# Kernel tuning notes

Measured on AMD Instinct MI355X. Metric: run time of the kernel, lower is better.

Reference implementation:

```python
import jax, jax.numpy as jnp
import numpy as np

L = 12      # n_blocks
H = 12      # n_heads
V = 64      # val_dim
D = 768     # hidden_d (token dim)
MLP = 3072  # MLP_dim
NP = 14     # n_patches per side
PS = 16     # patch size
C = 3       # channels
NC = 1000   # num_classes
EPS = 1e-5  # LayerNorm eps


def pos_embeddings(S, d):
    # result[i,j] = sin(i/10000**(j/d)) if j even else cos(i/10000**((j-1)/d))
    i = jnp.arange(S, dtype=jnp.float32)[:, None]
    j = jnp.arange(d, dtype=jnp.float32)[None, :]
    angle = i / jnp.power(10000.0, (j - (j % 2)) / d)
    even = (jnp.arange(d) % 2) == 0
    return jnp.where(even[None, :], jnp.sin(angle), jnp.cos(angle))


def patchify(images):
    # [n,C,H,W] -> [n, NP*NP, C*PS*PS], patch flattened in (c, ph, pw) order
    n = images.shape[0]
    x = images.reshape(n, C, NP, PS, NP, PS)
    x = x.transpose(0, 2, 4, 1, 3, 5)  # n, i, j, c, ps, ps
    return x.reshape(n, NP * NP, C * PS * PS)


def layernorm(x, w, b):
    m = jnp.mean(x, axis=-1, keepdims=True)
    v = jnp.var(x, axis=-1, keepdims=True)
    return (x - m) * jax.lax.rsqrt(v + EPS) * w + b


def setup_inputs() -> dict:
    key = jax.random.key(0)
    ks = jax.random.split(key, 10)
    s = lambda k, shape, scale=0.02: jax.random.normal(k, shape, jnp.float32) * scale
    return {
        "images": jax.random.normal(ks[0], (32, C, NP * PS, NP * PS), jnp.float32),
        "W_map": s(ks[1], (C * PS * PS, D)),          # linear_mapper (no bias)
        "class_token": s(ks[2], (1, D), 1.0),
        "pos_emb": pos_embeddings(NP * NP + 1, D),     # buffer
        "ln1_w": jnp.ones((L, D)), "ln1_b": jnp.zeros((L, D)),
        "qkv_w": s(ks[3], (L, D, 3 * H * V)),          # to_qkv (no bias)
        "merge_w": s(ks[4], (L, H * V, D)),            # Merge (no bias)
        "ln2_w": jnp.ones((L, D)), "ln2_b": jnp.zeros((L, D)),
        "mlp_w1": s(ks[5], (L, D, MLP)), "mlp_b1": jnp.zeros((L, MLP)),
        "mlp_w2": s(ks[6], (L, MLP, D)), "mlp_b2": jnp.zeros((L, D)),
        "head_w": s(ks[7], (D, NC)), "head_b": jnp.zeros((NC,)),
    }


def reference(images, W_map, class_token, pos_emb, ln1_w, ln1_b, qkv_w,
              merge_w, ln2_w, ln2_b, mlp_w1, mlp_b1, mlp_w2, mlp_b2,
              head_w, head_b):
    n = images.shape[0]
    tokens = patchify(images) @ W_map                              # [n, P, D]
    tokens = jnp.concatenate([jnp.broadcast_to(class_token, (n, 1, D)), tokens], axis=1)
    x = tokens + pos_emb                                           # [n, P+1, D]

    def block(x, p):
        l1w, l1b, qw, mw, l2w, l2b, w1, b1, w2, b2 = p
        h = layernorm(x, l1w, l1b)
        # rearrange 'b p (h v k) -> k b h p v' (k innermost factor)
        qkv = (h @ qw).reshape(n, -1, H, V, 3)
        q, k, v = qkv[..., 0], qkv[..., 1], qkv[..., 2]            # [n, P+1, H, V]
        attn = jnp.einsum('bihd,bjhd->bhij', q, k) * (V ** -0.5)
        attn = jax.nn.softmax(attn, axis=-1)
        o = jnp.einsum('bhij,bjhd->bihd', attn, v).reshape(n, -1, H * V)
        x = x + o @ mw
        h2 = layernorm(x, l2w, l2b)
        x = x + (jax.nn.gelu(h2 @ w1 + b1, approximate=False) @ w2 + b2)
        return x, None

    x, _ = jax.lax.scan(block, x, (ln1_w, ln1_b, qkv_w, merge_w,
                                   ln2_w, ln2_b, mlp_w1, mlp_b1, mlp_w2, mlp_b2))
    return jax.nn.softmax(x[:, 0] @ head_w + head_b, axis=-1)      # [n, NC]
```

## Files before the change

kernel.cpp:

```cpp
#include <hip/hip_runtime.h>
#include <math.h>

#define NIMG 32
#define NP2  196
#define PTOK 197
#define DIM  768
#define NH   12
#define VD   64
#define MLPD 3072
#define ROWS (NIMG*PTOK)
#define PROWS (NIMG*NP2)
#define MPAD 6400
#define PSTR 208
#define BHN (NIMG*NH)

typedef float f32x4 __attribute__((ext_vector_type(4)));
typedef short bf16x8 __attribute__((ext_vector_type(8)));
typedef unsigned short u16x8 __attribute__((ext_vector_type(8)));
typedef unsigned short u16x4 __attribute__((ext_vector_type(4)));

__device__ __forceinline__ unsigned short f2bf(float x) {
    unsigned int u = __float_as_uint(x);
    return (unsigned short)((u + 0x7FFFu + ((u >> 16) & 1u)) >> 16);
}
__device__ __forceinline__ float bfhi(unsigned short h) {
    return __uint_as_float(((unsigned int)h) << 16);
}
__device__ __forceinline__ void glds16(const unsigned short* g, unsigned short* l) {
    __builtin_amdgcn_global_load_lds(
        (const __attribute__((address_space(1))) unsigned int*)g,
        (__attribute__((address_space(3))) unsigned int*)l, 16, 0, 0);
}

__global__ __launch_bounds__(256) void patchify_kernel(const float* __restrict__ img,
                                                       unsigned short* __restrict__ ph,
                                                       unsigned short* __restrict__ pl)
{
    int idx = blockIdx.x * 256 + threadIdx.x;
    if (idx >= PROWS * DIM) return;
    int row = idx / DIM, kk = idx % DIM;
    int b = row / NP2, p = row % NP2;
    int i = p / 14, j = p % 14;
    int c = kk >> 8, r = kk & 255;
    int pr = r >> 4, pw = r & 15;
    float v = img[(((size_t)b*3 + c)*224 + i*16 + pr)*224 + j*16 + pw];
    unsigned short hi = f2bf(v);
    ph[idx] = hi;
    pl[idx] = f2bf(v - bfhi(hi));
}

__global__ __launch_bounds__(256) void class_pos_kernel(const float* __restrict__ ct,
                                                        const float* __restrict__ pos,
                                                        float* __restrict__ x)
{
    int idx = blockIdx.x * 256 + threadIdx.x;
    if (idx >= NIMG * DIM) return;
    int b = idx / DIM, d = idx % DIM;
    x[(size_t)b * PTOK * DIM + d] = ct[d] + pos[d];
}

__device__ __forceinline__ void conv_body(const float* __restrict__ W,
    unsigned short* __restrict__ Bh, unsigned short* __restrict__ Bl, int K, int N)
{
    int idx = blockIdx.x * 256 + threadIdx.x;
    if (idx >= N * (K >> 5)) return;
    int kb = idx / N;
    int n  = idx - kb * N;
    size_t off = (((size_t)(n >> 7) * (K >> 5) + kb) * 128 + (n & 127)) * 32;
    #pragma unroll
    for (int u = 0; u < 4; ++u) {
        u16x8 h, l;
        #pragma unroll
        for (int j = 0; j < 8; ++j) {
            float x = W[(size_t)(kb * 32 + u * 8 + j) * N + n];
            unsigned short hh = f2bf(x);
            h[j] = hh;
            l[j] = f2bf(x - bfhi(hh));
        }
        *(u16x8*)&Bh[off + u * 8] = h;
        *(u16x8*)&Bl[off + u * 8] = l;
    }
}

__global__ __launch_bounds__(256) void convert_one(const float* __restrict__ W,
    unsigned short* __restrict__ Bh, unsigned short* __restrict__ Bl, int K, int N)
{
    conv_body(W, Bh, Bl, K, N);
}

__global__ __launch_bounds__(256) void convert_layer(
    const float* __restrict__ qw, const float* __restrict__ mw,
    const float* __restrict__ w1, const float* __restrict__ w2,
    unsigned short* qh, unsigned short* ql, unsigned short* mh, unsigned short* ml,
    unsigned short* h1, unsigned short* l1, unsigned short* h2, unsigned short* l2)
{
    switch (blockIdx.y) {
        case 0: conv_body(qw, qh, ql, DIM, 3*NH*VD); break;
        case 1: conv_body(mw, mh, ml, DIM, DIM);     break;
        case 2: conv_body(w1, h1, l1, DIM, MLPD);    break;
        case 3: conv_body(w2, h2, l2, MLPD, DIM);    break;
    }
}

template<int MODE>
__global__ __launch_bounds__(512, 4) void mgemm(
    const unsigned short* __restrict__ Ah, const unsigned short* __restrict__ Al,
    const unsigned short* __restrict__ Bh, const unsigned short* __restrict__ Bl,
    float* __restrict__ C, int M, int N, int K, int gm, int gn,
    const float* __restrict__ bias, const float* __restrict__ res,
    const float* __restrict__ pos,
    unsigned int* __restrict__ qo, unsigned int* __restrict__ ko, unsigned int* __restrict__ vo,
    unsigned short* __restrict__ oph, unsigned short* __restrict__ opl)
{
    __shared__ unsigned short SAh[256 * 32];
    __shared__ unsigned short SAl[256 * 32];
    __shared__ unsigned short SBh[128 * 32];
    __shared__ unsigned short SBl[128 * 32];

    const int tid = threadIdx.x;
    const int nwg = gm * gn;
    const int q = nwg >> 3, r = nwg & 7;
    const int xcd = blockIdx.x & 7, li = blockIdx.x >> 3;
    const int seq = xcd * q + (xcd < r ? xcd : r) + li;
    const int mt = seq / gn, nt = seq - mt * gn;
    const int m0 = mt * 256, n0 = nt * 128;

    const int wave = tid >> 6, lane = tid & 63;
    const int wm = (wave >> 1) * 64, wn = (wave & 1) * 64;
    const int lr = lane & 15, lg = lane >> 4;

    const int r0 = tid >> 2, sl = tid & 3;
    const int s0 = sl ^ ((r0 >> 1) & 3);
    const size_t aoff0 = (size_t)(m0 + r0) * K + s0 * 8;
    const size_t aoff1 = (size_t)(m0 + r0 + 128) * K + s0 * 8;
    const size_t boff0 = (size_t)(n0 >> 7) * (K >> 5) * 4096 + (size_t)r0 * 32 + s0 * 8;

    int aro[4], bro[4];
    #pragma unroll
    for (int i = 0; i < 4; ++i) {
        int rowA = wm + i * 16 + lr;
        aro[i] = rowA * 32 + ((lg ^ ((rowA >> 1) & 3)) * 8);
        int rowB = wn + i * 16 + lr;
        bro[i] = rowB * 32 + ((lg ^ ((rowB >> 1) & 3)) * 8);
    }

    f32x4 acc[4][4];
    #pragma unroll
    for (int i = 0; i < 4; ++i)
        #pragma unroll
        for (int j = 0; j < 4; ++j)
            #pragma unroll
            for (int e = 0; e < 4; ++e) acc[i][j][e] = 0.f;

    const int kSteps = K >> 5;
    #pragma unroll 1
    for (int ks = 0; ks < kSteps; ++ks) {
        __syncthreads();
        const size_t ak = (size_t)ks * 32;
        const size_t bk = (size_t)ks * 4096;
        glds16(Ah + aoff0 + ak, SAh + tid * 8);
        glds16(Ah + aoff1 + ak, SAh + 4096 + tid * 8);
        glds16(Al + aoff0 + ak, SAl + tid * 8);
        glds16(Al + aoff1 + ak, SAl + 4096 + tid * 8);
        glds16(Bh + boff0 + bk, SBh + tid * 8);
        glds16(Bl + boff0 + bk, SBl + tid * 8);
        __syncthreads();

        bf16x8 bfh[4], bfl[4];
        #pragma unroll
        for (int ni = 0; ni < 4; ++ni) {
            bfh[ni] = *(const bf16x8*)&SBh[bro[ni]];
            bfl[ni] = *(const bf16x8*)&SBl[bro[ni]];
        }
        #pragma unroll
        for (int mi = 0; mi < 4; ++mi) {
            bf16x8 afh = *(const bf16x8*)&SAh[aro[mi]];
            bf16x8 afl = *(const bf16x8*)&SAl[aro[mi]];
            #pragma unroll
            for (int ni = 0; ni < 4; ++ni) {
                acc[mi][ni] = __builtin_amdgcn_mfma_f32_16x16x32_bf16(afh, bfh[ni], acc[mi][ni], 0, 0, 0);
                acc[mi][ni] = __builtin_amdgcn_mfma_f32_16x16x32_bf16(afh, bfl[ni], acc[mi][ni], 0, 0, 0);
                acc[mi][ni] = __builtin_amdgcn_mfma_f32_16x16x32_bf16(afl, bfh[ni], acc[mi][ni], 0, 0, 0);
            }
        }
    }

    #pragma unroll
    for (int mi = 0; mi < 4; ++mi) {
        #pragma unroll
        for (int ni = 0; ni < 4; ++ni) {
            f32x4 v = acc[mi][ni];
            int c = n0 + wn + ni * 16 + lr;
            #pragma unroll
            for (int rr = 0; rr < 4; ++rr) {
                int r = m0 + wm + mi * 16 + lg * 4 + rr;
                if (r >= M) continue;
                float val = v[rr];
                if (MODE == 1) {
                    int b = r / NP2, p = r - b * NP2;
                    C[((size_t)b * PTOK + 1 + p) * DIM + c] = val + pos[(size_t)(p + 1) * DIM + c];
                } else if (MODE == 2) {
                    int b = r / PTOK, p = r - b * PTOK;
                    int t = c % 3, hv = c / 3;
                    int hd = hv >> 6, vv = hv & 63;
                    size_t bh = (size_t)b * NH + hd;
                    float sv = (t == 0) ? val * 0.125f : val;
                    unsigned short hi = f2bf(sv);
                    unsigned short lo = f2bf(sv - bfhi(hi));
                    unsigned int w32 = (unsigned int)hi | ((unsigned int)lo << 16);
                    if (t == 2) vo[(bh * 64 + vv) * PSTR + p] = w32;
                    else if (t == 0) qo[(bh * PSTR + p) * 64 + vv] = w32;
                    else ko[(bh * PSTR + p) * 64 + vv] = w32;
                } else if (MODE == 3) {
                    float tmp = val + bias[c];
                    float gel = 0.5f * tmp * (1.0f + erff(tmp * 0.70710678118654752f));
                    unsigned short hi = f2bf(gel);
                    oph[(size_t)r * N + c] = hi;
                    opl[(size_t)r * N + c] = f2bf(gel - bfhi(hi));
                } else if (MODE == 4) {
                    C[(size_t)r * N + c] = res[(size_t)r * N + c] + val;
                } else if (MODE == 5) {
                    C[(size_t)r * N + c] = res[(size_t)r * N + c] + val + bias[c];
                }
            }
        }
    }
}

__global__ __launch_bounds__(256) void ln_kernel(const float* __restrict__ x,
                                                 const float* __restrict__ w,
                                                 const float* __restrict__ b,
                                                 unsigned short* __restrict__ oh,
                                                 unsigned short* __restrict__ ol, int rows)
{
    int wave = threadIdx.x >> 6, lane = threadIdx.x & 63;
    int row = blockIdx.x * 4 + wave;
    if (row >= rows) return;
    const float* xr = x + (size_t)row * DIM;
    float vals[12];
    float sum = 0.f;
    #pragma unroll
    for (int u = 0; u < 12; ++u) { vals[u] = xr[u * 64 + lane]; sum += vals[u]; }
    #pragma unroll
    for (int off = 32; off; off >>= 1) sum += __shfl_xor(sum, off);
    float mean = sum * (1.f / DIM);
    float vs = 0.f;
    #pragma unroll
    for (int u = 0; u < 12; ++u) { float d = vals[u] - mean; vs += d * d; }
    #pragma unroll
    for (int off = 32; off; off >>= 1) vs += __shfl_xor(vs, off);
    float rstd = rsqrtf(vs * (1.f / DIM) + 1e-5f);
    #pragma unroll
    for (int u = 0; u < 12; ++u) {
        int d = u * 64 + lane;
        float v = (vals[u] - mean) * rstd * w[d] + b[d];
        unsigned short hi = f2bf(v);
        oh[(size_t)row * DIM + d] = hi;
        ol[(size_t)row * DIM + d] = f2bf(v - bfhi(hi));
    }
}

__global__ __launch_bounds__(256) void attn_mfma(
    const unsigned int* __restrict__ qp, const unsigned int* __restrict__ kp,
    const unsigned int* __restrict__ vtp,
    unsigned short* __restrict__ oh, unsigned short* __restrict__ ol)
{
    __shared__ unsigned short KVh[64 * 72];
    __shared__ unsigned short KVl[64 * 72];
    __shared__ unsigned short Ph[64 * 72];
    __shared__ unsigned short Pl[64 * 72];

    const int tid = threadIdx.x;
    const int w = tid >> 6, lane = tid & 63;
    const int l = lane & 15, g = lane >> 4;
    const int bh = blockIdx.y, q0 = blockIdx.x * 64;
    const int b = bh / NH, hd = bh - b * NH;

    int qrow = q0 + 16 * w + l;
    if (qrow >= PTOK) qrow = 0;
    const unsigned int* qbase = qp + ((size_t)bh * PSTR + qrow) * 64;
    bf16x8 qAh[2], qAl[2];
    #pragma unroll
    for (int ks = 0; ks < 2; ++ks) {
        const unsigned int* p = qbase + 32 * ks + 8 * g;
        uint4 a = *(const uint4*)p;
        uint4 c = *(const uint4*)(p + 4);
        bf16x8 h8, l8;
        h8[0]=(short)a.x; h8[1]=(short)a.y; h8[2]=(short)a.z; h8[3]=(short)a.w;
        h8[4]=(short)c.x; h8[5]=(short)c.y; h8[6]=(short)c.z; h8[7]=(short)c.w;
        l8[0]=(short)(a.x>>16); l8[1]=(short)(a.y>>16); l8[2]=(short)(a.z>>16); l8[3]=(short)(a.w>>16);
        l8[4]=(short)(c.x>>16); l8[5]=(short)(c.y>>16); l8[6]=(short)(c.z>>16); l8[7]=(short)(c.w>>16);
        qAh[ks] = h8; qAl[ks] = l8;
    }

    f32x4 s[13];
    #pragma unroll
    for (int t = 0; t < 13; ++t)
        #pragma unroll
        for (int e = 0; e < 4; ++e) s[t][e] = 0.f;

    for (int c = 0; c < 4; ++c) {
        __syncthreads();
        const int rows = (c < 3) ? 64 : 16;
        for (int u = tid; u < rows * 16; u += 256) {
            int r = u >> 4, cc = u & 15;
            int j = c * 64 + r;
            uint4 wv = make_uint4(0, 0, 0, 0);
            if (j < PTOK) wv = *(const uint4*)(kp + ((size_t)bh * PSTR + j) * 64 + cc * 4);
            u16x4 h4, l4;
            h4[0]=(unsigned short)wv.x; h4[1]=(unsigned short)wv.y;
            h4[2]=(unsigned short)wv.z; h4[3]=(unsigned short)wv.w;
            l4[0]=(unsigned short)(wv.x>>16); l4[1]=(unsigned short)(wv.y>>16);
            l4[2]=(unsigned short)(wv.z>>16); l4[3]=(unsigned short)(wv.w>>16);
            *(u16x4*)&KVh[r * 72 + cc * 4] = h4;
            *(u16x4*)&KVl[r * 72 + cc * 4] = l4;
        }
        __syncthreads();
        const int tc = (c < 3) ? 4 : 1;
        for (int t = 0; t < tc; ++t) {
            int ti = c * 4 + t;
            #pragma unroll
            for (int ks = 0; ks < 2; ++ks) {
                bf16x8 kh = *(const bf16x8*)&KVh[(16 * t + l) * 72 + 32 * ks + 8 * g];
                bf16x8 kl = *(const bf16x8*)&KVl[(16 * t + l) * 72 + 32 * ks + 8 * g];
                s[ti] = __builtin_amdgcn_mfma_f32_16x16x32_bf16(qAh[ks], kh, s[ti], 0, 0, 0);
                s[ti] = __builtin_amdgcn_mfma_f32_16x16x32_bf16(qAh[ks], kl, s[ti], 0, 0, 0);
                s[ti] = __builtin_amdgcn_mfma_f32_16x16x32_bf16(qAl[ks], kh, s[ti], 0, 0, 0);
            }
        }
    }

    if (l >= 5) {
        #pragma unroll
        for (int e = 0; e < 4; ++e) s[12][e] = -1e30f;
    }

    float mx[4], rs[4];
    #pragma unroll
    for (int e = 0; e < 4; ++e) {
        float m = s[0][e];
        #pragma unroll
        for (int t = 1; t < 13; ++t) m = fmaxf(m, s[t][e]);
        #pragma unroll
        for (int off = 1; off < 16; off <<= 1) m = fmaxf(m, __shfl_xor(m, off));
        mx[e] = m;
    }
    #pragma unroll
    for (int e = 0; e < 4; ++e) {
        float sum = 0.f;
        #pragma unroll
        for (int t = 0; t < 13; ++t) {
            float p = __expf(s[t][e] - mx[e]);
            s[t][e] = p;
            sum += p;
        }
        #pragma unroll
        for (int off = 1; off < 16; off <<= 1) sum += __shfl_xor(sum, off);
        rs[e] = 1.f / sum;
    }

    f32x4 o[4];
    #pragma unroll
    for (int t = 0; t < 4; ++t)
        #pragma unroll
        for (int e = 0; e < 4; ++e) o[t][e] = 0.f;

    for (int c = 0; c < 4; ++c) {
        __syncthreads();
        const int cols = (c < 3) ? 64 : 32;
        const int cpr = cols >> 2;
        for (int u = tid; u < 64 * cpr; u += 256) {
            int r = u / cpr, cc = u % cpr;
            int jbase = c * 64 + cc * 4;
            uint4 wv;
            if (c < 3) {
                wv = *(const uint4*)(vtp + ((size_t)bh * 64 + r) * PSTR + jbase);
            } else {
                unsigned int t0 = (jbase + 0 < PTOK) ? vtp[((size_t)bh * 64 + r) * PSTR + jbase + 0] : 0u;
                unsigned int t1 = (jbase + 1 < PTOK) ? vtp[((size_t)bh * 64 + r) * PSTR + jbase + 1] : 0u;
                unsigned int t2 = (jbase + 2 < PTOK) ? vtp[((size_t)bh * 64 + r) * PSTR + jbase + 2] : 0u;
                unsigned int t3 = (jbase + 3 < PTOK) ? vtp[((size_t)bh * 64 + r) * PSTR + jbase + 3] : 0u;
                wv = make_uint4(t0, t1, t2, t3);
            }
            u16x4 h4, l4;
            h4[0]=(unsigned short)wv.x; h4[1]=(unsigned short)wv.y;
            h4[2]=(unsigned short)wv.z; h4[3]=(unsigned short)wv.w;
            l4[0]=(unsigned short)(wv.x>>16); l4[1]=(unsigned short)(wv.y>>16);
            l4[2]=(unsigned short)(wv.z>>16); l4[3]=(unsigned short)(wv.w>>16);
            *(u16x4*)&KVh[r * 72 + cc * 4] = h4;
            *(u16x4*)&KVl[r * 72 + cc * 4] = l4;
        }
        const int tc = (c < 3) ? 4 : 1;
        for (int t = 0; t < tc; ++t) {
            int ti = c * 4 + t;
            #pragma unroll
            for (int e = 0; e < 4; ++e) {
                int row = 16 * w + 4 * g + e, col = 16 * t + l;
                float pv = s[ti][e];
                unsigned short hi = f2bf(pv);
                Ph[row * 72 + col] = hi;
                Pl[row * 72 + col] = f2bf(pv - bfhi(hi));
            }
        }
        __syncthreads();
        const int ksn = (c < 3) ? 2 : 1;
        for (int ks = 0; ks < ksn; ++ks) {
            bf16x8 pa_h = *(const bf16x8*)&Ph[(16 * w + l) * 72 + 32 * ks + 8 * g];
            bf16x8 pa_l = *(const bf16x8*)&Pl[(16 * w + l) * 72 + 32 * ks + 8 * g];
            #pragma unroll
            for (int tv = 0; tv < 4; ++tv) {
                bf16x8 vh = *(const bf16x8*)&KVh[(16 * tv + l) * 72 + 32 * ks + 8 * g];
                bf16x8 vl = *(const bf16x8*)&KVl[(16 * tv + l) * 72 + 32 * ks + 8 * g];
                o[tv] = __builtin_amdgcn_mfma_f32_16x16x32_bf16(pa_h, vh, o[tv], 0, 0, 0);
                o[tv] = __builtin_amdgcn_mfma_f32_16x16x32_bf16(pa_h, vl, o[tv], 0, 0, 0);
                o[tv] = __builtin_amdgcn_mfma_f32_16x16x32_bf16(pa_l, vh, o[tv], 0, 0, 0);
            }
        }
    }

    #pragma unroll
    for (int tv = 0; tv < 4; ++tv) {
        #pragma unroll
        for (int e = 0; e < 4; ++e) {
            int q = q0 + 16 * w + 4 * g + e;
            if (q < PTOK) {
                float v = o[tv][e] * rs[e];
                size_t idx = ((size_t)(b * PTOK + q)) * DIM + hd * 64 + 16 * tv + l;
                unsigned short hi = f2bf(v);
                oh[idx] = hi;
                ol[idx] = f2bf(v - bfhi(hi));
            }
        }
    }
}

__global__ __launch_bounds__(256) void head_kernel(const float* __restrict__ x,
                                                   const float* __restrict__ W,
                                                   const float* __restrict__ bias,
                                                   float* __restrict__ out)
{
    __shared__ __align__(16) float xl[DIM];
    __shared__ float red[4];
    int b = blockIdx.x;
    const float* xr = x + (size_t)b * PTOK * DIM;
    for (int idx = threadIdx.x; idx < DIM; idx += 256) xl[idx] = xr[idx];
    __syncthreads();

    float logit[4];
    #pragma unroll
    for (int u = 0; u < 4; ++u) {
        int c = threadIdx.x + u * 256;
        float acc = (c < 1000) ? bias[c] : -INFINITY;
        if (c < 1000) {
            for (int k = 0; k < DIM; k += 4) {
                float4 xv = *(const float4*)&xl[k];
                acc += xv.x * W[(size_t)k * 1000 + c]
                     + xv.y * W[(size_t)(k + 1) * 1000 + c]
                     + xv.z * W[(size_t)(k + 2) * 1000 + c]
                     + xv.w * W[(size_t)(k + 3) * 1000 + c];
            }
        }
        logit[u] = acc;
    }
    int lane = threadIdx.x & 63, wv = threadIdx.x >> 6;
    float m = fmaxf(fmaxf(logit[0], logit[1]), fmaxf(logit[2], logit[3]));
    #pragma unroll
    for (int off = 32; off; off >>= 1) m = fmaxf(m, __shfl_xor(m, off));
    if (lane == 0) red[wv] = m;
    __syncthreads();
    m = fmaxf(fmaxf(red[0], red[1]), fmaxf(red[2], red[3]));

    float p[4]; float sum = 0.f;
    #pragma unroll
    for (int u = 0; u < 4; ++u) {
        int c = threadIdx.x + u * 256;
        p[u] = (c < 1000) ? expf(logit[u] - m) : 0.f;
        sum += p[u];
    }
    #pragma unroll
    for (int off = 32; off; off >>= 1) sum += __shfl_xor(sum, off);
    __syncthreads();
    if (lane == 0) red[wv] = sum;
    __syncthreads();
    float inv = 1.f / (red[0] + red[1] + red[2] + red[3]);
    #pragma unroll
    for (int u = 0; u < 4; ++u) {
        int c = threadIdx.x + u * 256;
        if (c < 1000) out[(size_t)b * 1000 + c] = p[u] * inv;
    }
}

extern "C" void kernel_launch(void* const* d_in, const int* in_sizes, int n_in,
                              void* d_out, int out_size, void* d_ws, size_t ws_size,
                              hipStream_t stream)
{
    const float* images  = (const float*)d_in[0];
    const float* W_map   = (const float*)d_in[1];
    const float* ct      = (const float*)d_in[2];
    const float* pos     = (const float*)d_in[3];
    const float* ln1_w   = (const float*)d_in[4];
    const float* ln1_b   = (const float*)d_in[5];
    const float* qkv_w   = (const float*)d_in[6];
    const float* merge_w = (const float*)d_in[7];
    const float* ln2_w   = (const float*)d_in[8];
    const float* ln2_b   = (const float*)d_in[9];
    const float* mlp_w1  = (const float*)d_in[10];
    const float* mlp_b1  = (const float*)d_in[11];
    const float* mlp_w2  = (const float*)d_in[12];
    const float* mlp_b2  = (const float*)d_in[13];
    const float* head_w  = (const float*)d_in[14];
    const float* head_b  = (const float*)d_in[15];
    float* out = (float*)d_out;

    float* ws = (float*)d_ws;
    const size_t XE   = (size_t)ROWS * DIM;
    const size_t PLND = (size_t)MPAD * DIM;
    const size_t GPL  = (size_t)MPAD * MLPD;

    float* x = ws;
    unsigned short* hh = (unsigned short*)(x + XE);
    unsigned short* hl = hh + PLND;
    unsigned short* oh = hl + PLND;
    unsigned short* ol = oh + PLND;
    unsigned short* gh = ol + PLND;
    unsigned short* gl = gh + GPL;

    const size_t PL = (size_t)BHN * PSTR * 64;
    unsigned int* qpl = (unsigned int*)gh;
    unsigned int* kpl = qpl + PL;
    unsigned int* vtp = kpl + PL;
    unsigned short* pph = gh;
    unsigned short* ppl = pph + PLND;

    unsigned short* wb = gl + GPL;
    const size_t qkvE = (size_t)DIM * 2304;
    const size_t mgE  = (size_t)DIM * DIM;
    const size_t m1E  = (size_t)DIM * MLPD;
    const size_t m2E  = (size_t)MLPD * DIM;
    unsigned short* qh  = wb;
    unsigned short* ql  = qh  + qkvE;
    unsigned short* mh  = ql  + qkvE;
    unsigned short* ml  = mh  + mgE;
    unsigned short* h1  = ml  + mgE;
    unsigned short* l1  = h1  + m1E;
    unsigned short* h2  = l1  + m1E;
    unsigned short* l2  = h2  + m2E;
    unsigned short* wmh = l2  + m2E;
    unsigned short* wml = wmh + mgE;

    patchify_kernel<<<(PROWS * DIM + 255) / 256, 256, 0, stream>>>(images, pph, ppl);
    class_pos_kernel<<<(NIMG * DIM + 255) / 256, 256, 0, stream>>>(ct, pos, x);
    convert_one<<<(DIM * (DIM / 32) + 255) / 256, 256, 0, stream>>>(W_map, wmh, wml, DIM, DIM);

    const int gm = 25;
    mgemm<1><<<gm * 6, 512, 0, stream>>>(
        pph, ppl, wmh, wml, x, PROWS, DIM, DIM, gm, 6,
        nullptr, nullptr, pos, nullptr, nullptr, nullptr, nullptr, nullptr);

    for (int l = 0; l < 12; ++l) {
        convert_layer<<<dim3(288, 4), 256, 0, stream>>>(
            qkv_w + (size_t)l * qkvE, merge_w + (size_t)l * mgE,
            mlp_w1 + (size_t)l * m1E, mlp_w2 + (size_t)l * m2E,
            qh, ql, mh, ml, h1, l1, h2, l2);
        ln_kernel<<<(ROWS + 3) / 4, 256, 0, stream>>>(x, ln1_w + l * DIM, ln1_b + l * DIM, hh, hl, ROWS);
        mgemm<2><<<gm * 18, 512, 0, stream>>>(
            hh, hl, qh, ql, nullptr, ROWS, 2304, DIM, gm, 18,
            nullptr, nullptr, nullptr, qpl, kpl, vtp, nullptr, nullptr);
        attn_mfma<<<dim3(4, BHN), 256, 0, stream>>>(qpl, kpl, vtp, oh, ol);
        mgemm<4><<<gm * 6, 512, 0, stream>>>(
            oh, ol, mh, ml, x, ROWS, DIM, DIM, gm, 6,
            nullptr, x, nullptr, nullptr, nullptr, nullptr, nullptr, nullptr);
        ln_kernel<<<(ROWS + 3) / 4, 256, 0, stream>>>(x, ln2_w + l * DIM, ln2_b + l * DIM, hh, hl, ROWS);
        mgemm<3><<<gm * 24, 512, 0, stream>>>(
            hh, hl, h1, l1, nullptr, ROWS, MLPD, DIM, gm, 24,
            mlp_b1 + (size_t)l * MLPD, nullptr, nullptr, nullptr, nullptr, nullptr, gh, gl);
        mgemm<5><<<gm * 6, 512, 0, stream>>>(
            gh, gl, h2, l2, x, ROWS, DIM, MLPD, gm, 6,
            mlp_b2 + (size_t)l * DIM, x, nullptr, nullptr, nullptr, nullptr, nullptr, nullptr);
    }
    head_kernel<<<NIMG, 256, 0, stream>>>(x, head_w, head_b, out);
}
```

Baseline: 6.507 ms.

## Double-buffer LDS in split-bf16 GEMM and shrink tile to 128x128 with 256 threads

The main GEMM kernel changes from a 256x128 tile with 512 threads and a single LDS buffer to a 128x128 tile with 256 threads and two LDS buffers. Global-to-LDS loads for the next K step are issued before the MFMA work on the current step, with one wait and barrier per step instead of two barriers. The goal is to hide global load latency behind MFMA work, and the smaller tiles give more workgroups for better CU fill. In exchange, each workgroup reuses less data, and the K-loop unrolled by two assumes an even number of K steps.

Result: no change. 6.427 ms (-1.2%).

```diff
diff --git a/kernel.cpp b/kernel.cpp
--- a/kernel.cpp
+++ b/kernel.cpp
@@ -103,7 +103,7 @@
 }
 
 template<int MODE>
-__global__ __launch_bounds__(512, 4) void mgemm(
+__global__ __launch_bounds__(256, 2) void mgemm(
     const unsigned short* __restrict__ Ah, const unsigned short* __restrict__ Al,
     const unsigned short* __restrict__ Bh, const unsigned short* __restrict__ Bl,
     float* __restrict__ C, int M, int N, int K, int gm, int gn,
@@ -112,10 +112,10 @@
     unsigned int* __restrict__ qo, unsigned int* __restrict__ ko, unsigned int* __restrict__ vo,
     unsigned short* __restrict__ oph, unsigned short* __restrict__ opl)
 {
-    __shared__ unsigned short SAh[256 * 32];
-    __shared__ unsigned short SAl[256 * 32];
-    __shared__ unsigned short SBh[128 * 32];
-    __shared__ unsigned short SBl[128 * 32];
+    __shared__ unsigned short SAh[2 * 4096];
+    __shared__ unsigned short SAl[2 * 4096];
+    __shared__ unsigned short SBh[2 * 4096];
+    __shared__ unsigned short SBl[2 * 4096];
 
     const int tid = threadIdx.x;
     const int nwg = gm * gn;
@@ -123,7 +123,7 @@
     const int xcd = blockIdx.x & 7, li = blockIdx.x >> 3;
     const int seq = xcd * q + (xcd < r ? xcd : r) + li;
     const int mt = seq / gn, nt = seq - mt * gn;
-    const int m0 = mt * 256, n0 = nt * 128;
+    const int m0 = mt * 128, n0 = nt * 128;
 
     const int wave = tid >> 6, lane = tid & 63;
     const int wm = (wave >> 1) * 64, wn = (wave & 1) * 64;
@@ -132,7 +132,7 @@
     const int r0 = tid >> 2, sl = tid & 3;
     const int s0 = sl ^ ((r0 >> 1) & 3);
     const size_t aoff0 = (size_t)(m0 + r0) * K + s0 * 8;
-    const size_t aoff1 = (size_t)(m0 + r0 + 128) * K + s0 * 8;
+    const size_t aoff1 = (size_t)(m0 + r0 + 64) * K + s0 * 8;
     const size_t boff0 = (size_t)(n0 >> 7) * (K >> 5) * 4096 + (size_t)r0 * 32 + s0 * 8;
 
     int aro[4], bro[4];
@@ -152,38 +152,68 @@
             #pragma unroll
             for (int e = 0; e < 4; ++e) acc[i][j][e] = 0.f;
 
+#define STAGE(KS, B) do { \
+    const size_t _ak = (size_t)(KS) * 32; \
+    const size_t _bk = (size_t)(KS) * 4096; \
+    unsigned short* _sah = SAh + (B) * 4096; \
+    unsigned short* _sal = SAl + (B) * 4096; \
+    unsigned short* _sbh = SBh + (B) * 4096; \
+    unsigned short* _sbl = SBl + (B) * 4096; \
+    glds16(Ah + aoff0 + _ak, _sah + tid * 8); \
+    glds16(Ah + aoff1 + _ak, _sah + 2048 + tid * 8); \
+    glds16(Al + aoff0 + _ak, _sal + tid * 8); \
+    glds16(Al + aoff1 + _ak, _sal + 2048 + tid * 8); \
+    glds16(Bh + boff0 + _bk, _sbh + tid * 8); \
+    glds16(Bh + boff0 + _bk + 2048, _sbh + 2048 + tid * 8); \
+    glds16(Bl + boff0 + _bk, _sbl + tid * 8); \
+    glds16(Bl + boff0 + _bk + 2048, _sbl + 2048 + tid * 8); \
+} while (0)
+
+#define COMPUTE(B) do { \
+    const unsigned short* _sah = SAh + (B) * 4096; \
+    const unsigned short* _sal = SAl + (B) * 4096; \
+    const unsigned short* _sbh = SBh + (B) * 4096; \
+    const unsigned short* _sbl = SBl + (B) * 4096; \
+    bf16x8 bfh[4], bfl[4]; \
+    _Pragma("unroll") \
+    for (int ni = 0; ni < 4; ++ni) { \
+        bfh[ni] = *(const bf16x8*)&_sbh[bro[ni]]; \
+        bfl[ni] = *(const bf16x8*)&_sbl[bro[ni]]; \
+    } \
+    _Pragma("unroll") \
+    for (int mi = 0; mi < 4; ++mi) { \
+        bf16x8 afh = *(const bf16x8*)&_sah[aro[mi]]; \
+        bf16x8 afl = *(const bf16x8*)&_sal[aro[mi]]; \
+        _Pragma("unroll") \
+        for (int ni = 0; ni < 4; ++ni) { \
+            acc[mi][ni] = __builtin_amdgcn_mfma_f32_16x16x32_bf16(afh, bfh[ni], acc[mi][ni], 0, 0, 0); \
+            acc[mi][ni] = __builtin_amdgcn_mfma_f32_16x16x32_bf16(afh, bfl[ni], acc[mi][ni], 0, 0, 0); \
+            acc[mi][ni] = __builtin_amdgcn_mfma_f32_16x16x32_bf16(afl, bfh[ni], acc[mi][ni], 0, 0, 0); \
+        } \
+    } \
+} while (0)
+
+#define WAITBAR do { \
+    asm volatile("s_waitcnt vmcnt(0)" ::: "memory"); \
+    __builtin_amdgcn_s_barrier(); \
+} while (0)
+
     const int kSteps = K >> 5;
+    STAGE(0, 0);
+    WAITBAR;
+
     #pragma unroll 1
-    for (int ks = 0; ks < kSteps; ++ks) {
-        __syncthreads();
-        const size_t ak = (size_t)ks * 32;
-        const size_t bk = (size_t)ks * 4096;
-        glds16(Ah + aoff0 + ak, SAh + tid * 8);
-        glds16(Ah + aoff1 + ak, SAh + 4096 + tid * 8);
-        glds16(Al + aoff0 + ak, SAl + tid * 8);
-        glds16(Al + aoff1 + ak, SAl + 4096 + tid * 8);
-        glds16(Bh + boff0 + bk, SBh + tid * 8);
-        glds16(Bl + boff0 + bk, SBl + tid * 8);
-        __syncthreads();
-
-        bf16x8 bfh[4], bfl[4];
-        #pragma unroll
-        for (int ni = 0; ni < 4; ++ni) {
-            bfh[ni] = *(const bf16x8*)&SBh[bro[ni]];
-            bfl[ni] = *(const bf16x8*)&SBl[bro[ni]];
-        }
-        #pragma unroll
-        for (int mi = 0; mi < 4; ++mi) {
-            bf16x8 afh = *(const bf16x8*)&SAh[aro[mi]];
-            bf16x8 afl = *(const bf16x8*)&SAl[aro[mi]];
-            #pragma unroll
-            for (int ni = 0; ni < 4; ++ni) {
-                acc[mi][ni] = __builtin_amdgcn_mfma_f32_16x16x32_bf16(afh, bfh[ni], acc[mi][ni], 0, 0, 0);
-                acc[mi][ni] = __builtin_amdgcn_mfma_f32_16x16x32_bf16(afh, bfl[ni], acc[mi][ni], 0, 0, 0);
-                acc[mi][ni] = __builtin_amdgcn_mfma_f32_16x16x32_bf16(afl, bfh[ni], acc[mi][ni], 0, 0, 0);
-            }
-        }
-    }
+    for (int ks = 0; ks < kSteps; ks += 2) {
+        STAGE(ks + 1, 1);
+        COMPUTE(0);
+        WAITBAR;
+        if (ks + 2 < kSteps) STAGE(ks + 2, 0);
+        COMPUTE(1);
+        WAITBAR;
+    }
+#undef STAGE
+#undef COMPUTE
+#undef WAITBAR
 
     #pragma unroll
     for (int mi = 0; mi < 4; ++mi) {
@@ -552,29 +582,30 @@
     class_pos_kernel<<<(NIMG * DIM + 255) / 256, 256, 0, stream>>>(ct, pos, x);
     convert_one<<<(DIM * (DIM / 32) + 255) / 256, 256, 0, stream>>>(W_map, wmh, wml, DIM, DIM);
 
-    const int gm = 25;
-    mgemm<1><<<gm * 6, 512, 0, stream>>>(
-        pph, ppl, wmh, wml, x, PROWS, DIM, DIM, gm, 6,
+    const int gme = 49;
+    mgemm<1><<<gme * 6, 256, 0, stream>>>(
+        pph, ppl, wmh, wml, x, PROWS, DIM, DIM, gme, 6,
         nullptr, nullptr, pos, nullptr, nullptr, nullptr, nullptr, nullptr);
 
+    const int gm = 50;
     for (int l = 0; l < 12; ++l) {
         convert_layer<<<dim3(288, 4), 256, 0, stream>>>(
             qkv_w + (size_t)l * qkvE, merge_w + (size_t)l * mgE,
             mlp_w1 + (size_t)l * m1E, mlp_w2 + (size_t)l * m2E,
             qh, ql, mh, ml, h1, l1, h2, l2);
         ln_kernel<<<(ROWS + 3) / 4, 256, 0, stream>>>(x, ln1_w + l * DIM, ln1_b + l * DIM, hh, hl, ROWS);
-        mgemm<2><<<gm * 18, 512, 0, stream>>>(
+        mgemm<2><<<gm * 18, 256, 0, stream>>>(
             hh, hl, qh, ql, nullptr, ROWS, 2304, DIM, gm, 18,
             nullptr, nullptr, nullptr, qpl, kpl, vtp, nullptr, nullptr);
         attn_mfma<<<dim3(4, BHN), 256, 0, stream>>>(qpl, kpl, vtp, oh, ol);
-        mgemm<4><<<gm * 6, 512, 0, stream>>>(
+        mgemm<4><<<gm * 6, 256, 0, stream>>>(
             oh, ol, mh, ml, x, ROWS, DIM, DIM, gm, 6,
             nullptr, x, nullptr, nullptr, nullptr, nullptr, nullptr, nullptr);
         ln_kernel<<<(ROWS + 3) / 4, 256, 0, stream>>>(x, ln2_w + l * DIM, ln2_b + l * DIM, hh, hl, ROWS);
-        mgemm<3><<<gm * 24, 512, 0, stream>>>(
+        mgemm<3><<<gm * 24, 256, 0, stream>>>(
             hh, hl, h1, l1, nullptr, ROWS, MLPD, DIM, gm, 24,
             mlp_b1 + (size_t)l * MLPD, nullptr, nullptr, nullptr, nullptr, nullptr, gh, gl);
-        mgemm<5><<<gm * 6, 512, 0, stream>>>(
+        mgemm<5><<<gm * 6, 256, 0, stream>>>(
             gh, gl, h2, l2, x, ROWS, DIM, MLPD, gm, 6,
             mlp_b2 + (size_t)l * DIM, x, nullptr, nullptr, nullptr, nullptr, nullptr, nullptr);
     }
```

## Add double-buffered 256x256 GEMM for wide layers, shrink narrow GEMM tiles

Applied to the files above, without the earlier changes.

Adds a new 512-thread GEMM kernel with 256x256 tiles and double-buffered LDS staging. The QKV and MLP-up projections now use it, giving each B tile more reuse and overlapping global-to-LDS loads with MFMA compute. The N=768 GEMMs (patch embed, merge, MLP-down) switch to 256-thread 128x128 tiles, doubling the workgroup count to fill more CUs. The large tile uses 128 KB of LDS and many accumulator registers, which limits occupancy. The smaller tile lowers per-block data reuse.

After: 6.182 ms. 5.0% less time.

```diff
diff --git a/kernel.cpp b/kernel.cpp
--- a/kernel.cpp
+++ b/kernel.cpp
@@ -103,7 +103,43 @@
 }
 
 template<int MODE>
-__global__ __launch_bounds__(512, 4) void mgemm(
+__device__ __forceinline__ void epi_store(
+    int r, int c, float val, float* __restrict__ C, int M, int N,
+    const float* __restrict__ bias, const float* __restrict__ res,
+    const float* __restrict__ pos,
+    unsigned int* __restrict__ qo, unsigned int* __restrict__ ko, unsigned int* __restrict__ vo,
+    unsigned short* __restrict__ oph, unsigned short* __restrict__ opl)
+{
+    if (MODE == 1) {
+        int b = r / NP2, p = r - b * NP2;
+        C[((size_t)b * PTOK + 1 + p) * DIM + c] = val + pos[(size_t)(p + 1) * DIM + c];
+    } else if (MODE == 2) {
+        int b = r / PTOK, p = r - b * PTOK;
+        int t = c % 3, hv = c / 3;
+        int hd = hv >> 6, vv = hv & 63;
+        size_t bh = (size_t)b * NH + hd;
+        float sv = (t == 0) ? val * 0.125f : val;
+        unsigned short hi = f2bf(sv);
+        unsigned short lo = f2bf(sv - bfhi(hi));
+        unsigned int w32 = (unsigned int)hi | ((unsigned int)lo << 16);
+        if (t == 2) vo[(bh * 64 + vv) * PSTR + p] = w32;
+        else if (t == 0) qo[(bh * PSTR + p) * 64 + vv] = w32;
+        else ko[(bh * PSTR + p) * 64 + vv] = w32;
+    } else if (MODE == 3) {
+        float tmp = val + bias[c];
+        float gel = 0.5f * tmp * (1.0f + erff(tmp * 0.70710678118654752f));
+        unsigned short hi = f2bf(gel);
+        oph[(size_t)r * N + c] = hi;
+        opl[(size_t)r * N + c] = f2bf(gel - bfhi(hi));
+    } else if (MODE == 4) {
+        C[(size_t)r * N + c] = res[(size_t)r * N + c] + val;
+    } else if (MODE == 5) {
+        C[(size_t)r * N + c] = res[(size_t)r * N + c] + val + bias[c];
+    }
+}
+
+template<int MODE>
+__global__ __launch_bounds__(256, 4) void mgemm(
     const unsigned short* __restrict__ Ah, const unsigned short* __restrict__ Al,
     const unsigned short* __restrict__ Bh, const unsigned short* __restrict__ Bl,
     float* __restrict__ C, int M, int N, int K, int gm, int gn,
@@ -112,10 +148,10 @@
     unsigned int* __restrict__ qo, unsigned int* __restrict__ ko, unsigned int* __restrict__ vo,
     unsigned short* __restrict__ oph, unsigned short* __restrict__ opl)
 {
-    __shared__ unsigned short SAh[256 * 32];
-    __shared__ unsigned short SAl[256 * 32];
-    __shared__ unsigned short SBh[128 * 32];
-    __shared__ unsigned short SBl[128 * 32];
+    __shared__ unsigned short SAh[4096];
+    __shared__ unsigned short SAl[4096];
+    __shared__ unsigned short SBh[4096];
+    __shared__ unsigned short SBl[4096];
 
     const int tid = threadIdx.x;
     const int nwg = gm * gn;
@@ -123,7 +159,7 @@
     const int xcd = blockIdx.x & 7, li = blockIdx.x >> 3;
     const int seq = xcd * q + (xcd < r ? xcd : r) + li;
     const int mt = seq / gn, nt = seq - mt * gn;
-    const int m0 = mt * 256, n0 = nt * 128;
+    const int m0 = mt * 128, n0 = nt * 128;
 
     const int wave = tid >> 6, lane = tid & 63;
     const int wm = (wave >> 1) * 64, wn = (wave & 1) * 64;
@@ -132,7 +168,7 @@
     const int r0 = tid >> 2, sl = tid & 3;
     const int s0 = sl ^ ((r0 >> 1) & 3);
     const size_t aoff0 = (size_t)(m0 + r0) * K + s0 * 8;
-    const size_t aoff1 = (size_t)(m0 + r0 + 128) * K + s0 * 8;
+    const size_t aoff1 = (size_t)(m0 + r0 + 64) * K + s0 * 8;
     const size_t boff0 = (size_t)(n0 >> 7) * (K >> 5) * 4096 + (size_t)r0 * 32 + s0 * 8;
 
     int aro[4], bro[4];
@@ -159,11 +195,13 @@
         const size_t ak = (size_t)ks * 32;
         const size_t bk = (size_t)ks * 4096;
         glds16(Ah + aoff0 + ak, SAh + tid * 8);
-        glds16(Ah + aoff1 + ak, SAh + 4096 + tid * 8);
+        glds16(Ah + aoff1 + ak, SAh + 2048 + tid * 8);
         glds16(Al + aoff0 + ak, SAl + tid * 8);
-        glds16(Al + aoff1 + ak, SAl + 4096 + tid * 8);
+        glds16(Al + aoff1 + ak, SAl + 2048 + tid * 8);
         glds16(Bh + boff0 + bk, SBh + tid * 8);
+        glds16(Bh + boff0 + bk + 2048, SBh + 2048 + tid * 8);
         glds16(Bl + boff0 + bk, SBl + tid * 8);
+        glds16(Bl + boff0 + bk + 2048, SBl + 2048 + tid * 8);
         __syncthreads();
 
         bf16x8 bfh[4], bfl[4];
@@ -193,35 +231,143 @@
             int c = n0 + wn + ni * 16 + lr;
             #pragma unroll
             for (int rr = 0; rr < 4; ++rr) {
-                int r = m0 + wm + mi * 16 + lg * 4 + rr;
-                if (r >= M) continue;
-                float val = v[rr];
-                if (MODE == 1) {
-                    int b = r / NP2, p = r - b * NP2;
-                    C[((size_t)b * PTOK + 1 + p) * DIM + c] = val + pos[(size_t)(p + 1) * DIM + c];
-                } else if (MODE == 2) {
-                    int b = r / PTOK, p = r - b * PTOK;
-                    int t = c % 3, hv = c / 3;
-                    int hd = hv >> 6, vv = hv & 63;
-                    size_t bh = (size_t)b * NH + hd;
-                    float sv = (t == 0) ? val * 0.125f : val;
-                    unsigned short hi = f2bf(sv);
-                    unsigned short lo = f2bf(sv - bfhi(hi));
-                    unsigned int w32 = (unsigned int)hi | ((unsigned int)lo << 16);
-                    if (t == 2) vo[(bh * 64 + vv) * PSTR + p] = w32;
-                    else if (t == 0) qo[(bh * PSTR + p) * 64 + vv] = w32;
-                    else ko[(bh * PSTR + p) * 64 + vv] = w32;
-                } else if (MODE == 3) {
-                    float tmp = val + bias[c];
-                    float gel = 0.5f * tmp * (1.0f + erff(tmp * 0.70710678118654752f));
-                    unsigned short hi = f2bf(gel);
-                    oph[(size_t)r * N + c] = hi;
-                    opl[(size_t)r * N + c] = f2bf(gel - bfhi(hi));
-                } else if (MODE == 4) {
-                    C[(size_t)r * N + c] = res[(size_t)r * N + c] + val;
-                } else if (MODE == 5) {
-                    C[(size_t)r * N + c] = res[(size_t)r * N + c] + val + bias[c];
-                }
+                int rr2 = m0 + wm + mi * 16 + lg * 4 + rr;
+                if (rr2 >= M) continue;
+                epi_store<MODE>(rr2, c, v[rr], C, M, N, bias, res, pos, qo, ko, vo, oph, opl);
+            }
+        }
+    }
+}
+
+template<int MODE>
+__global__ __launch_bounds__(512, 2) void mgemm2(
+    const unsigned short* __restrict__ Ah, const unsigned short* __restrict__ Al,
+    const unsigned short* __restrict__ Bh, const unsigned short* __restrict__ Bl,
+    float* __restrict__ C, int M, int N, int K, int gm, int gn,
+    const float* __restrict__ bias, const float* __restrict__ res,
+    const float* __restrict__ pos,
+    unsigned int* __restrict__ qo, unsigned int* __restrict__ ko, unsigned int* __restrict__ vo,
+    unsigned short* __restrict__ oph, unsigned short* __restrict__ opl)
+{
+    __shared__ unsigned short SAh[2 * 8192];
+    __shared__ unsigned short SAl[2 * 8192];
+    __shared__ unsigned short SBh[2 * 8192];
+    __shared__ unsigned short SBl[2 * 8192];
+
+    const int tid = threadIdx.x;
+    const int nwg = gm * gn;
+    const int q = nwg >> 3, r = nwg & 7;
+    const int xcd = blockIdx.x & 7, li = blockIdx.x >> 3;
+    const int seq = xcd * q + (xcd < r ? xcd : r) + li;
+    const int mt = seq / gn, nt = seq - mt * gn;
+    const int m0 = mt * 256, n0 = nt * 256;
+
+    const int wave = tid >> 6, lane = tid & 63;
+    const int wm = (wave >> 2) * 128, wn = (wave & 3) * 64;
+    const int lr = lane & 15, lg = lane >> 4;
+
+    const int r0 = tid >> 2, sl = tid & 3;
+    const int s0 = sl ^ ((r0 >> 1) & 3);
+    const size_t aoff0 = (size_t)(m0 + r0) * K + s0 * 8;
+    const size_t aoff1 = (size_t)(m0 + r0 + 128) * K + s0 * 8;
+    const size_t bstep = (size_t)(K >> 5) * 4096;
+    const size_t bo0 = (size_t)(n0 >> 7) * bstep + (size_t)r0 * 32 + s0 * 8;
+    const size_t bo1 = bo0 + bstep;
+
+    int aro[8], bro[4];
+    #pragma unroll
+    for (int i = 0; i < 8; ++i) {
+        int rowA = wm + i * 16 + lr;
+        aro[i] = rowA * 32 + ((lg ^ ((rowA >> 1) & 3)) * 8);
+    }
+    #pragma unroll
+    for (int i = 0; i < 4; ++i) {
+        int rowB = wn + i * 16 + lr;
+        bro[i] = rowB * 32 + ((lg ^ ((rowB >> 1) & 3)) * 8);
+    }
+
+    f32x4 acc[8][4];
+    #pragma unroll
+    for (int i = 0; i < 8; ++i)
+        #pragma unroll
+        for (int j = 0; j < 4; ++j)
+            #pragma unroll
+            for (int e = 0; e < 4; ++e) acc[i][j][e] = 0.f;
+
+#define STAGE2(KS, B) do { \
+    const size_t _ak = (size_t)(KS) * 32; \
+    const size_t _bk = (size_t)(KS) * 4096; \
+    unsigned short* _sah = SAh + (B) * 8192; \
+    unsigned short* _sal = SAl + (B) * 8192; \
+    unsigned short* _sbh = SBh + (B) * 8192; \
+    unsigned short* _sbl = SBl + (B) * 8192; \
+    glds16(Ah + aoff0 + _ak, _sah + tid * 8); \
+    glds16(Ah + aoff1 + _ak, _sah + 4096 + tid * 8); \
+    glds16(Al + aoff0 + _ak, _sal + tid * 8); \
+    glds16(Al + aoff1 + _ak, _sal + 4096 + tid * 8); \
+    glds16(Bh + bo0 + _bk, _sbh + tid * 8); \
+    glds16(Bh + bo1 + _bk, _sbh + 4096 + tid * 8); \
+    glds16(Bl + bo0 + _bk, _sbl + tid * 8); \
+    glds16(Bl + bo1 + _bk, _sbl + 4096 + tid * 8); \
+} while (0)
+
+#define COMPUTE2(B) do { \
+    const unsigned short* _sah = SAh + (B) * 8192; \
+    const unsigned short* _sal = SAl + (B) * 8192; \
+    const unsigned short* _sbh = SBh + (B) * 8192; \
+    const unsigned short* _sbl = SBl + (B) * 8192; \
+    bf16x8 bfh[4], bfl[4]; \
+    _Pragma("unroll") \
+    for (int ni = 0; ni < 4; ++ni) { \
+        bfh[ni] = *(const bf16x8*)&_sbh[bro[ni]]; \
+        bfl[ni] = *(const bf16x8*)&_sbl[bro[ni]]; \
+    } \
+    _Pragma("unroll") \
+    for (int mi = 0; mi < 8; ++mi) { \
+        bf16x8 afh = *(const bf16x8*)&_sah[aro[mi]]; \
+        bf16x8 afl = *(const bf16x8*)&_sal[aro[mi]]; \
+        _Pragma("unroll") \
+        for (int ni = 0; ni < 4; ++ni) { \
+            acc[mi][ni] = __builtin_amdgcn_mfma_f32_16x16x32_bf16(afh, bfh[ni], acc[mi][ni], 0, 0, 0); \
+            acc[mi][ni] = __builtin_amdgcn_mfma_f32_16x16x32_bf16(afh, bfl[ni], acc[mi][ni], 0, 0, 0); \
+            acc[mi][ni] = __builtin_amdgcn_mfma_f32_16x16x32_bf16(afl, bfh[ni], acc[mi][ni], 0, 0, 0); \
+        } \
+    } \
+} while (0)
+
+#define WAITBAR2 do { \
+    asm volatile("s_waitcnt vmcnt(0)" ::: "memory"); \
+    __builtin_amdgcn_s_barrier(); \
+} while (0)
+
+    const int kSteps = K >> 5;
+    STAGE2(0, 0);
+    WAITBAR2;
+
+    #pragma unroll 1
+    for (int ks = 0; ks < kSteps; ks += 2) {
+        STAGE2(ks + 1, 1);
+        COMPUTE2(0);
+        WAITBAR2;
+        if (ks + 2 < kSteps) STAGE2(ks + 2, 0);
+        COMPUTE2(1);
+        WAITBAR2;
+    }
+#undef STAGE2
+#undef COMPUTE2
+#undef WAITBAR2
+
+    #pragma unroll
+    for (int mi = 0; mi < 8; ++mi) {
+        #pragma unroll
+        for (int ni = 0; ni < 4; ++ni) {
+            f32x4 v = acc[mi][ni];
+            int c = n0 + wn + ni * 16 + lr;
+            #pragma unroll
+            for (int rr = 0; rr < 4; ++rr) {
+                int rr2 = m0 + wm + mi * 16 + lg * 4 + rr;
+                if (rr2 >= M) continue;
+                epi_store<MODE>(rr2, c, v[rr], C, M, N, bias, res, pos, qo, ko, vo, oph, opl);
             }
         }
     }
@@ -552,29 +698,31 @@
     class_pos_kernel<<<(NIMG * DIM + 255) / 256, 256, 0, stream>>>(ct, pos, x);
     convert_one<<<(DIM * (DIM / 32) + 255) / 256, 256, 0, stream>>>(W_map, wmh, wml, DIM, DIM);
 
-    const int gm = 25;
-    mgemm<1><<<gm * 6, 512, 0, stream>>>(
-        pph, ppl, wmh, wml, x, PROWS, DIM, DIM, gm, 6,
+    const int gme = 49;
+    mgemm<1><<<gme * 6, 256, 0, stream>>>(
+        pph, ppl, wmh, wml, x, PROWS, DIM, DIM, gme, 6,
         nullptr, nullptr, pos, nullptr, nullptr, nullptr, nullptr, nullptr);
 
+    const int gm = 50;
+    const int gm2 = 25;
     for (int l = 0; l < 12; ++l) {
         convert_layer<<<dim3(288, 4), 256, 0, stream>>>(
             qkv_w + (size_t)l * qkvE, merge_w + (size_t)l * mgE,
             mlp_w1 + (size_t)l * m1E, mlp_w2 + (size_t)l * m2E,
             qh, ql, mh, ml, h1, l1, h2, l2);
         ln_kernel<<<(ROWS + 3) / 4, 256, 0, stream>>>(x, ln1_w + l * DIM, ln1_b + l * DIM, hh, hl, ROWS);
-        mgemm<2><<<gm * 18, 512, 0, stream>>>(
-            hh, hl, qh, ql, nullptr, ROWS, 2304, DIM, gm, 18,
+        mgemm2<2><<<gm2 * 9, 512, 0, stream>>>(
+            hh, hl, qh, ql, nullptr, ROWS, 2304, DIM, gm2, 9,
             nullptr, nullptr, nullptr, qpl, kpl, vtp, nullptr, nullptr);
         attn_mfma<<<dim3(4, BHN), 256, 0, stream>>>(qpl, kpl, vtp, oh, ol);
-        mgemm<4><<<gm * 6, 512, 0, stream>>>(
+        mgemm<4><<<gm * 6, 256, 0, stream>>>(
             oh, ol, mh, ml, x, ROWS, DIM, DIM, gm, 6,
             nullptr, x, nullptr, nullptr, nullptr, nullptr, nullptr, nullptr);
         ln_kernel<<<(ROWS + 3) / 4, 256, 0, stream>>>(x, ln2_w + l * DIM, ln2_b + l * DIM, hh, hl, ROWS);
-        mgemm<3><<<gm * 24, 512, 0, stream>>>(
-            hh, hl, h1, l1, nullptr, ROWS, MLPD, DIM, gm, 24,
+        mgemm2<3><<<gm2 * 12, 512, 0, stream>>>(
+            hh, hl, h1, l1, nullptr, ROWS, MLPD, DIM, gm2, 12,
             mlp_b1 + (size_t)l * MLPD, nullptr, nullptr, nullptr, nullptr, nullptr, gh, gl);
-        mgemm<5><<<gm * 6, 512, 0, stream>>>(
+        mgemm<5><<<gm * 6, 256, 0, stream>>>(
             gh, gl, h2, l2, x, ROWS, DIM, MLPD, gm, 6,
             mlp_b2 + (size_t)l * DIM, x, nullptr, nullptr, nullptr, nullptr, nullptr, nullptr);
     }
```
